# Performance work log

Hardware: AMD Instinct MI355X
Metric: run time of the kernel (lower is better)

Reference implementation:

```python
import jax, jax.numpy as jnp
import numpy as np

N = 100000  # nodes


def gcn_conv(x, src, dst, deg_inv_sqrt, W, b):
    h = x @ W  # transform first (smaller feature dim for propagation when F_out < F_in)
    norm = deg_inv_sqrt[src] * deg_inv_sqrt[dst]  # [E]
    msg = h[src] * norm[:, None]  # gather + scale
    return jax.ops.segment_sum(msg, dst, num_segments=N) + b


def setup_inputs() -> dict:
    key = jax.random.key(0)
    k1, k2, k3, k4, k5 = jax.random.split(key, 5)
    E = 3200000
    x = jax.random.normal(k1, (N, 512), dtype=jnp.float32)
    edge_index = jax.random.randint(k2, (2, E), 0, N, dtype=jnp.int64)
    W1 = jax.random.normal(k3, (512, 16), dtype=jnp.float32) * (1.0 / np.sqrt(512))
    b1 = jnp.zeros((16,), dtype=jnp.float32)
    W2 = jax.random.normal(k4, (16, 64), dtype=jnp.float32) * (1.0 / np.sqrt(16))
    b2 = jnp.zeros((64,), dtype=jnp.float32)
    return {"x": x, "edge_index": edge_index, "W1": W1, "b1": b1, "W2": W2, "b2": b2}


def reference(x, edge_index, W1, b1, W2, b2):
    # add self-loops (PyG GCNConv default add_self_loops=True)
    loops = jnp.arange(N, dtype=edge_index.dtype)
    src = jnp.concatenate([edge_index[0], loops])
    dst = jnp.concatenate([edge_index[1], loops])
    # symmetric normalization: deg computed on destination (in-degree incl. self-loop)
    deg = jax.ops.segment_sum(jnp.ones_like(dst, dtype=x.dtype), dst, num_segments=N)
    deg_inv_sqrt = jnp.where(deg > 0, jax.lax.rsqrt(jnp.maximum(deg, 1.0)), 0.0)

    h = jax.nn.relu(gcn_conv(x, src, dst, deg_inv_sqrt, W1, b1))
    out = gcn_conv(h, src, dst, deg_inv_sqrt, W2, b2)
    return jax.nn.log_softmax(out, axis=1)
```

## Files before the change

### kernel.cpp

```cpp
#include <hip/hip_runtime.h>

#define FIN 512
#define FMID 16
#define FOUT 64

typedef __attribute__((ext_vector_type(8))) short bf8_t;
typedef __attribute__((ext_vector_type(4))) float f32x4_t;

__device__ __forceinline__ unsigned short f2bf_rne(float f) {
  unsigned u = __float_as_uint(f);
  return (unsigned short)((u + 0x7FFFu + ((u >> 16) & 1u)) >> 16);
}
__device__ __forceinline__ float bf2f(unsigned short h) {
  return __uint_as_float(((unsigned)h) << 16);
}


#define CHUNK 8192

__global__ __launch_bounds__(256) void k_bhist(const int* __restrict__ dst,
                                               int* __restrict__ gtot, int E, int nbuck) {
  __shared__ int hist[1024];
  const int t = threadIdx.x;
  const int base = blockIdx.x * CHUNK;
  const int nloc = min(CHUNK, E - base);
  for (int i = t; i < nbuck; i += 256) hist[i] = 0;
  __syncthreads();
  const int nv = nloc & ~3;
  for (int i = t * 4; i < nv; i += 1024) {
    int4 d = *(const int4*)(dst + base + i);
    atomicAdd(&hist[d.x >> 8], 1);
    atomicAdd(&hist[d.y >> 8], 1);
    atomicAdd(&hist[d.z >> 8], 1);
    atomicAdd(&hist[d.w >> 8], 1);
  }
  if (t == 0)
    for (int i = nv; i < nloc; ++i) atomicAdd(&hist[dst[base + i] >> 8], 1);
  __syncthreads();
  for (int i = t; i < nbuck; i += 256) {
    int c = hist[i];
    if (c) atomicAdd(&gtot[i], c);
  }
}

__global__ __launch_bounds__(1024) void k_bscan(int* __restrict__ gbase,
                                                int* __restrict__ gcur,
                                                int* __restrict__ rowstart,
                                                int E, int n, int nbuck) {
  __shared__ int sm[1024];
  int t = threadIdx.x;
  int v = (t < nbuck) ? gbase[t] : 0;
  sm[t] = v;
  __syncthreads();
  for (int off = 1; off < 1024; off <<= 1) {
    int a = (t >= off) ? sm[t - off] : 0;
    __syncthreads();
    sm[t] += a;
    __syncthreads();
  }
  int excl = sm[t] - v;
  if (t < nbuck) {
    gbase[t] = excl;
    gcur[t] = excl;
  }
  if (t == 0) {
    gbase[nbuck] = E;
    rowstart[n] = E;
  }
}

__global__ __launch_bounds__(256) void k_bucketA(const int* __restrict__ src,
                                                 const int* __restrict__ dst,
                                                 int* __restrict__ gcur,
                                                 int* __restrict__ packed,
                                                 int E, int nbuck) {
  __shared__ int hist[1024];
  const int t = threadIdx.x;
  const int base = blockIdx.x * CHUNK;
  const int nloc = min(CHUNK, E - base);
  for (int i = t; i < nbuck; i += 256) hist[i] = 0;
  __syncthreads();
  const int nv = nloc & ~3;
  for (int i = t * 4; i < nv; i += 1024) {
    int4 d = *(const int4*)(dst + base + i);
    atomicAdd(&hist[d.x >> 8], 1);
    atomicAdd(&hist[d.y >> 8], 1);
    atomicAdd(&hist[d.z >> 8], 1);
    atomicAdd(&hist[d.w >> 8], 1);
  }
  if (t == 0)
    for (int i = nv; i < nloc; ++i) atomicAdd(&hist[dst[base + i] >> 8], 1);
  __syncthreads();
  for (int i = t; i < nbuck; i += 256) {
    int c = hist[i];
    hist[i] = c ? atomicAdd(&gcur[i], c) : 0;
  }
  __syncthreads();
  for (int i = t * 4; i < nv; i += 1024) {
    int4 d = *(const int4*)(dst + base + i);
    int4 s = *(const int4*)(src + base + i);
    int p0 = atomicAdd(&hist[d.x >> 8], 1);
    int p1 = atomicAdd(&hist[d.y >> 8], 1);
    int p2 = atomicAdd(&hist[d.z >> 8], 1);
    int p3 = atomicAdd(&hist[d.w >> 8], 1);
    packed[p0] = (s.x << 8) | (d.x & 255);
    packed[p1] = (s.y << 8) | (d.y & 255);
    packed[p2] = (s.z << 8) | (d.z & 255);
    packed[p3] = (s.w << 8) | (d.w & 255);
  }
  if (t == 0)
    for (int i = nv; i < nloc; ++i) {
      int d = dst[base + i], s = src[base + i];
      int p = atomicAdd(&hist[d >> 8], 1);
      packed[p] = (s << 8) | (d & 255);
    }
}

__global__ __launch_bounds__(256) void k_bucketB(const int* __restrict__ packed,
                                                 const int* __restrict__ gbase,
                                                 int* __restrict__ rowstart,
                                                 float* __restrict__ dis,
                                                 int* __restrict__ csr, int n) {
  __shared__ int cnt[256];
  __shared__ int cur[256];
  const int b = blockIdx.x;
  const int t = threadIdx.x;
  const int beg = gbase[b], end = gbase[b + 1];
  cnt[t] = 0;
  __syncthreads();
  for (int i = beg + t; i < end; i += 256) atomicAdd(&cnt[packed[i] & 255], 1);
  __syncthreads();
  int v = cnt[t];
  cur[t] = v;
  __syncthreads();
  for (int off = 1; off < 256; off <<= 1) {
    int a = (t >= off) ? cur[t - off] : 0;
    __syncthreads();
    cur[t] += a;
    __syncthreads();
  }
  int excl = cur[t] - v;
  int node = (b << 8) + t;
  if (node < n) {
    rowstart[node] = beg + excl;
    dis[node] = rsqrtf((float)v + 1.0f);
  }
  __syncthreads();
  cur[t] = beg + excl;
  __syncthreads();
  for (int i = beg + t; i < end; i += 256) {
    int p = packed[i];
    int pos = atomicAdd(&cur[p & 255], 1);
    csr[pos] = p >> 8;
  }
}


__global__ __launch_bounds__(256) void k_gemm1(const float* __restrict__ x,
                                               const float* __restrict__ W1,
                                               const float* __restrict__ dis,
                                               float* __restrict__ hs, int n,
                                               int ntiles) {
  __shared__ short wb_hi[16][64][8];
  __shared__ short wb_lo[16][64][8];
  for (int e = threadIdx.x; e < FIN * FMID; e += 256) {
    int k = e >> 4, j = e & 15;
    int ks = k >> 5, kk = k & 31;
    int L = ((kk >> 3) << 4) + j, i = kk & 7;
    float f = W1[e];
    unsigned short h = f2bf_rne(f);
    wb_hi[ks][L][i] = (short)h;
    wb_lo[ks][L][i] = (short)f2bf_rne(f - bf2f(h));
  }
  __syncthreads();
  const int lane = threadIdx.x & 63;
  const int wid  = threadIdx.x >> 6;
  const int rloc = lane & 15;
  const int q    = lane >> 4;
  for (int tile = blockIdx.x * 4 + wid; tile < ntiles; tile += gridDim.x * 4) {
    int row = tile * 16 + rloc;
    const float4* xr = (const float4*)(x + (size_t)(row < n ? row : n - 1) * FIN);
    f32x4_t acc = {0.f, 0.f, 0.f, 0.f};
#pragma unroll 4
    for (int ks = 0; ks < 16; ++ks) {
      float4 v0 = xr[ks * 8 + q * 2];
      float4 v1 = xr[ks * 8 + q * 2 + 1];
      float fv[8] = {v0.x, v0.y, v0.z, v0.w, v1.x, v1.y, v1.z, v1.w};
      bf8_t ah, al;
#pragma unroll
      for (int i = 0; i < 8; ++i) {
        unsigned short h = f2bf_rne(fv[i]);
        ah[i] = (short)h;
        al[i] = (short)f2bf_rne(fv[i] - bf2f(h));
      }
      bf8_t bh = *(const bf8_t*)&wb_hi[ks][lane][0];
      bf8_t bl = *(const bf8_t*)&wb_lo[ks][lane][0];
      acc = __builtin_amdgcn_mfma_f32_16x16x32_bf16(ah, bh, acc, 0, 0, 0);
      acc = __builtin_amdgcn_mfma_f32_16x16x32_bf16(al, bh, acc, 0, 0, 0);
      acc = __builtin_amdgcn_mfma_f32_16x16x32_bf16(ah, bl, acc, 0, 0, 0);
    }
    int nb = tile * 16 + q * 4;
#pragma unroll
    for (int r = 0; r < 4; ++r) {
      int node = nb + r;
      if (node < n) hs[(size_t)node * FMID + rloc] = acc[r] * dis[node];
    }
  }
}

template <bool RELU>
__global__ __launch_bounds__(256) void k_prop_csr(const float* __restrict__ hs,
                                                  const int* __restrict__ rowstart,
                                                  const int* __restrict__ csr,
                                                  const float* __restrict__ dis,
                                                  const float* __restrict__ bias,
                                                  float* __restrict__ outp, int n) {
  int t = blockIdx.x * blockDim.x + threadIdx.x;
  int node = t >> 4;
  if (node >= n) return;
  const int j = t & 15;
  const int g = j >> 2;
  const int c = j & 3;
  int beg = rowstart[node], end = rowstart[node + 1];
  float4 acc = make_float4(0.f, 0.f, 0.f, 0.f);
  if (g == 0) {
    float4 v = ((const float4*)(hs + (size_t)node * FMID))[c];
    acc.x += v.x; acc.y += v.y; acc.z += v.z; acc.w += v.w;
  }
  int i = beg;
  int stop = beg + ((end - beg) & ~15);
  for (; i < stop; i += 16) {
    int sv = csr[i + j];
#pragma unroll
    for (int k = 0; k < 4; ++k) {
      int sidx = __shfl(sv, k * 4 + g, 16);
      float4 v = ((const float4*)(hs + (size_t)sidx * FMID))[c];
      acc.x += v.x; acc.y += v.y; acc.z += v.z; acc.w += v.w;
    }
  }
  for (int u = 0; i < end; ++i, ++u) {
    int sidx = csr[i];
    if (g == (u & 3)) {
      float4 v = ((const float4*)(hs + (size_t)sidx * FMID))[c];
      acc.x += v.x; acc.y += v.y; acc.z += v.z; acc.w += v.w;
    }
  }
#pragma unroll
  for (int off = 4; off <= 8; off <<= 1) {
    acc.x += __shfl_xor(acc.x, off, 16);
    acc.y += __shfl_xor(acc.y, off, 16);
    acc.z += __shfl_xor(acc.z, off, 16);
    acc.w += __shfl_xor(acc.w, off, 16);
  }
  if (g == 0) {
    float dd = dis[node];
    float4 r;
    r.x = dd * acc.x; r.y = dd * acc.y; r.z = dd * acc.z; r.w = dd * acc.w;
    if (RELU) {
      float4 bb = ((const float4*)bias)[c];
      r.x = fmaxf(r.x + bb.x, 0.f) * dd;
      r.y = fmaxf(r.y + bb.y, 0.f) * dd;
      r.z = fmaxf(r.z + bb.z, 0.f) * dd;
      r.w = fmaxf(r.w + bb.w, 0.f) * dd;
    }
    ((float4*)(outp + (size_t)node * FMID))[c] = r;
  }
}

__global__ __launch_bounds__(256) void k_out(const float* __restrict__ a2,
                                             const float* __restrict__ W2,
                                             const float* __restrict__ b2,
                                             float* __restrict__ out, int n) {
  __shared__ float w[FMID * FOUT];
  for (int idx = threadIdx.x; idx < FMID * FOUT; idx += 256) w[idx] = W2[idx];
  __syncthreads();
  const int lane = threadIdx.x & 63;
  const int node = blockIdx.x * 4 + (threadIdx.x >> 6);
  if (node >= n) return;
  const float* ar = a2 + (size_t)node * FMID;
  float o = b2[lane];
#pragma unroll
  for (int k = 0; k < FMID; ++k) o += ar[k] * w[k * FOUT + lane];
  float m = o;
#pragma unroll
  for (int off = 32; off >= 1; off >>= 1) m = fmaxf(m, __shfl_xor(m, off));
  float e = __expf(o - m);
  float s = e;
#pragma unroll
  for (int off = 32; off >= 1; off >>= 1) s += __shfl_xor(s, off);
  out[(size_t)node * FOUT + lane] = o - m - __logf(s);
}


__global__ void k_deg_init(float* __restrict__ deg, int n) {
  int i = blockIdx.x * blockDim.x + threadIdx.x;
  if (i < n) deg[i] = 1.0f;
}
__global__ void k_deg_edges(const int* __restrict__ dst, float* __restrict__ deg, int E) {
  int e = blockIdx.x * blockDim.x + threadIdx.x;
  if (e < E) atomicAdd(&deg[dst[e]], 1.0f);
}
__global__ void k_deg_finish(float* __restrict__ deg, int n) {
  int i = blockIdx.x * blockDim.x + threadIdx.x;
  if (i < n) deg[i] = rsqrtf(deg[i]);
}
__global__ void k_selfloop_s(const float* __restrict__ hs, const float* __restrict__ dis,
                             float* __restrict__ a, int total16) {
  int t = blockIdx.x * blockDim.x + threadIdx.x;
  if (t < total16) a[t] = hs[t] * dis[t >> 4];
}
__global__ void k_prop_atomic(const float* __restrict__ hs, const int* __restrict__ src,
                              const int* __restrict__ dst, const float* __restrict__ dis,
                              float* __restrict__ outp, int E) {
  int t = blockIdx.x * blockDim.x + threadIdx.x;
  int e = t >> 4;
  if (e >= E) return;
  int jj = t & 15;
  int s = src[e], d = dst[e];
  atomicAdd(&outp[(size_t)d * FMID + jj], hs[(size_t)s * FMID + jj] * dis[d]);
}
__global__ void k_bias_relu_s(float* __restrict__ a, const float* __restrict__ b,
                              const float* __restrict__ dis, int total16) {
  int t = blockIdx.x * blockDim.x + threadIdx.x;
  if (t < total16) {
    float v = a[t] + b[t & 15];
    a[t] = (v > 0.f ? v : 0.f) * dis[t >> 4];
  }
}


extern "C" void kernel_launch(void* const* d_in, const int* in_sizes, int n_in,
                              void* d_out, int out_size, void* d_ws, size_t ws_size,
                              hipStream_t stream) {
  const float* x  = (const float*)d_in[0];
  const int* edge = (const int*)d_in[1];
  const float* W1 = (const float*)d_in[2];
  const float* b1 = (const float*)d_in[3];
  const float* W2 = (const float*)d_in[4];
  const float* b2 = (const float*)d_in[5];
  float* out = (float*)d_out;

  const int N = in_sizes[0] / FIN;
  const int E = in_sizes[1] / 2;
  const int* src = edge;
  const int* dst = edge + E;

  const int T = 256;
  const int t16n = N * FMID;
  const int ntiles = (N + 15) / 16;
  int gblocks = (ntiles + 3) / 4;
  if (gblocks > 2048) gblocks = 2048;

  const int nbuck = (N + 255) >> 8;
  const int nblkA = (E + CHUNK - 1) / CHUNK;

  size_t need_csr = ((size_t)33 * N + (size_t)(N + 1) + (size_t)(2 * nbuck + 1) +
                     (size_t)E) * 4;
  bool new_ok = (ws_size >= need_csr) && ((size_t)E <= (size_t)32 * N) &&
                (nbuck <= 1024) && ((size_t)N < (1u << 23));

  if (new_ok) {
    float* fbase = (float*)d_ws;
    float* dis  = fbase;
    float* buf0 = fbase + (size_t)N;
    float* buf1 = fbase + 17 * (size_t)N;
    int* packed   = (int*)buf0;
    int* ibase    = (int*)(fbase + 33 * (size_t)N);
    int* rowstart = ibase;
    int* gbase    = ibase + (size_t)N + 1;
    int* gcur     = gbase + nbuck + 1;
    int* csr      = gcur + nbuck;

    hipMemsetAsync(gbase, 0, (size_t)(nbuck + 1) * sizeof(int), stream);
    k_bhist  <<<nblkA, T, 0, stream>>>(dst, gbase, E, nbuck);
    k_bscan  <<<1, 1024, 0, stream>>>(gbase, gcur, rowstart, E, N, nbuck);
    k_bucketA<<<nblkA, T, 0, stream>>>(src, dst, gcur, packed, E, nbuck);
    k_bucketB<<<nbuck, T, 0, stream>>>(packed, gbase, rowstart, dis, csr, N);

    k_gemm1  <<<gblocks, T, 0, stream>>>(x, W1, dis, buf0, N, ntiles);

    const int PB = (t16n + T - 1) / T;
    k_prop_csr<true>  <<<PB, T, 0, stream>>>(buf0, rowstart, csr, dis, b1, buf1, N);
    k_prop_csr<false> <<<PB, T, 0, stream>>>(buf1, rowstart, csr, dis, b1, buf0, N);
    k_out    <<<(N + 3) / 4, T, 0, stream>>>(buf0, W2, b2, out, N);
  } else {
    float* f   = (float*)d_ws;
    float* dis = f;
    float* hs  = f + (size_t)N;
    float* a1  = f + 17 * (size_t)N;
    float* a2  = f + 33 * (size_t)N;
    const long te = (long)E * FMID;

    k_deg_init  <<<(N + T - 1) / T, T, 0, stream>>>(dis, N);
    k_deg_edges <<<(E + T - 1) / T, T, 0, stream>>>(dst, dis, E);
    k_deg_finish<<<(N + T - 1) / T, T, 0, stream>>>(dis, N);

    k_gemm1     <<<gblocks, T, 0, stream>>>(x, W1, dis, hs, N, ntiles);

    k_selfloop_s<<<(t16n + T - 1) / T, T, 0, stream>>>(hs, dis, a1, t16n);
    k_prop_atomic<<<(int)((te + T - 1) / T), T, 0, stream>>>(hs, src, dst, dis, a1, E);
    k_bias_relu_s<<<(t16n + T - 1) / T, T, 0, stream>>>(a1, b1, dis, t16n);

    k_selfloop_s<<<(t16n + T - 1) / T, T, 0, stream>>>(a1, dis, a2, t16n);
    k_prop_atomic<<<(int)((te + T - 1) / T), T, 0, stream>>>(a1, src, dst, dis, a2, E);

    k_out       <<<(N + 3) / 4, T, 0, stream>>>(a2, W2, b2, out, N);
  }
}
```

Before: 548.6 us.

## Switch CSR propagation to edge-parallel blocks with shared-memory atomic accumulation

The CSR array now keeps the packed (src<<8 | local dst) word, so propagation can run edge-parallel over each 64-node block's contiguous edge range. Each edge's 4-float chunk is gathered and added into a shared-memory accumulator with LDS atomics, replacing the node-per-16-lane loop that suffered from load imbalance and partial tail iterations. This trades warp divergence and degree imbalance for LDS atomic contention and extra block syncs. The output kernel also loads each node's 16 features as four float4 vectors instead of scalar reads.

```diff
diff --git a/kernel.cpp b/kernel.cpp
--- a/kernel.cpp
+++ b/kernel.cpp
@@ -151,7 +151,7 @@
   for (int i = beg + t; i < end; i += 256) {
     int p = packed[i];
     int pos = atomicAdd(&cur[p & 255], 1);
-    csr[pos] = p >> 8;
+    csr[pos] = p;
   }
 }
 
@@ -209,53 +209,47 @@
 }
 
 template <bool RELU>
-__global__ __launch_bounds__(256) void k_prop_csr(const float* __restrict__ hs,
-                                                  const int* __restrict__ rowstart,
-                                                  const int* __restrict__ csr,
-                                                  const float* __restrict__ dis,
-                                                  const float* __restrict__ bias,
-                                                  float* __restrict__ outp, int n) {
-  int t = blockIdx.x * blockDim.x + threadIdx.x;
-  int node = t >> 4;
-  if (node >= n) return;
-  const int j = t & 15;
-  const int g = j >> 2;
-  const int c = j & 3;
-  int beg = rowstart[node], end = rowstart[node + 1];
-  float4 acc = make_float4(0.f, 0.f, 0.f, 0.f);
-  if (g == 0) {
-    float4 v = ((const float4*)(hs + (size_t)node * FMID))[c];
-    acc.x += v.x; acc.y += v.y; acc.z += v.z; acc.w += v.w;
-  }
-  int i = beg;
-  int stop = beg + ((end - beg) & ~15);
-  for (; i < stop; i += 16) {
-    int sv = csr[i + j];
-#pragma unroll
-    for (int k = 0; k < 4; ++k) {
-      int sidx = __shfl(sv, k * 4 + g, 16);
-      float4 v = ((const float4*)(hs + (size_t)sidx * FMID))[c];
-      acc.x += v.x; acc.y += v.y; acc.z += v.z; acc.w += v.w;
+__global__ __launch_bounds__(256) void k_prop_ep(const float* __restrict__ hs,
+                                                 const int* __restrict__ rowstart,
+                                                 const int* __restrict__ csrp,
+                                                 const float* __restrict__ dis,
+                                                 const float* __restrict__ bias,
+                                                 float* __restrict__ outp, int n) {
+  __shared__ float acc[64][16];
+  const int t = threadIdx.x;
+  const int node0 = blockIdx.x * 64;
+  const int nl = t >> 2;
+  const int c  = t & 3;
+  const int node = node0 + nl;
+  float4 selfv = make_float4(0.f, 0.f, 0.f, 0.f);
+  if (node < n) selfv = ((const float4*)hs)[(size_t)node * 4 + c];
+  *(float4*)&acc[nl][c * 4] = selfv;
+  __syncthreads();
+  const int beg = rowstart[node0];
+  const int end = rowstart[min(node0 + 64, n)];
+  const int es = t >> 2;
+  for (int base = beg; base < end; base += 256) {
+#pragma unroll
+    for (int u = 0; u < 4; ++u) {
+      int i = base + u * 64 + es;
+      if (i < end) {
+        int p = csrp[i];
+        int s = p >> 8;
+        int dl = p & 63;
+        float4 v = ((const float4*)hs)[(size_t)s * 4 + c];
+        atomicAdd(&acc[dl][c * 4 + 0], v.x);
+        atomicAdd(&acc[dl][c * 4 + 1], v.y);
+        atomicAdd(&acc[dl][c * 4 + 2], v.z);
+        atomicAdd(&acc[dl][c * 4 + 3], v.w);
+      }
     }
   }
-  for (int u = 0; i < end; ++i, ++u) {
-    int sidx = csr[i];
-    if (g == (u & 3)) {
-      float4 v = ((const float4*)(hs + (size_t)sidx * FMID))[c];
-      acc.x += v.x; acc.y += v.y; acc.z += v.z; acc.w += v.w;
-    }
-  }
-#pragma unroll
-  for (int off = 4; off <= 8; off <<= 1) {
-    acc.x += __shfl_xor(acc.x, off, 16);
-    acc.y += __shfl_xor(acc.y, off, 16);
-    acc.z += __shfl_xor(acc.z, off, 16);
-    acc.w += __shfl_xor(acc.w, off, 16);
-  }
-  if (g == 0) {
+  __syncthreads();
+  if (node < n) {
     float dd = dis[node];
+    float4 a = *(const float4*)&acc[nl][c * 4];
     float4 r;
-    r.x = dd * acc.x; r.y = dd * acc.y; r.z = dd * acc.z; r.w = dd * acc.w;
+    r.x = dd * a.x; r.y = dd * a.y; r.z = dd * a.z; r.w = dd * a.w;
     if (RELU) {
       float4 bb = ((const float4*)bias)[c];
       r.x = fmaxf(r.x + bb.x, 0.f) * dd;
@@ -263,7 +257,7 @@
       r.z = fmaxf(r.z + bb.z, 0.f) * dd;
       r.w = fmaxf(r.w + bb.w, 0.f) * dd;
     }
-    ((float4*)(outp + (size_t)node * FMID))[c] = r;
+    ((float4*)outp)[(size_t)node * 4 + c] = r;
   }
 }
 
@@ -277,10 +271,13 @@
   const int lane = threadIdx.x & 63;
   const int node = blockIdx.x * 4 + (threadIdx.x >> 6);
   if (node >= n) return;
-  const float* ar = a2 + (size_t)node * FMID;
+  const float4* ar4 = (const float4*)(a2 + (size_t)node * FMID);
+  float4 q0 = ar4[0], q1 = ar4[1], q2 = ar4[2], q3 = ar4[3];
+  float av[16] = {q0.x, q0.y, q0.z, q0.w, q1.x, q1.y, q1.z, q1.w,
+                  q2.x, q2.y, q2.z, q2.w, q3.x, q3.y, q3.z, q3.w};
   float o = b2[lane];
 #pragma unroll
-  for (int k = 0; k < FMID; ++k) o += ar[k] * w[k * FOUT + lane];
+  for (int k = 0; k < FMID; ++k) o += av[k] * w[k * FOUT + lane];
   float m = o;
 #pragma unroll
   for (int off = 32; off >= 1; off >>= 1) m = fmaxf(m, __shfl_xor(m, off));
@@ -353,6 +350,7 @@
 
   const int nbuck = (N + 255) >> 8;
   const int nblkA = (E + CHUNK - 1) / CHUNK;
+  const int nblk64 = (N + 63) / 64;
 
   size_t need_csr = ((size_t)33 * N + (size_t)(N + 1) + (size_t)(2 * nbuck + 1) +
                      (size_t)E) * 4;
@@ -379,9 +377,8 @@
 
     k_gemm1  <<<gblocks, T, 0, stream>>>(x, W1, dis, buf0, N, ntiles);
 
-    const int PB = (t16n + T - 1) / T;
-    k_prop_csr<true>  <<<PB, T, 0, stream>>>(buf0, rowstart, csr, dis, b1, buf1, N);
-    k_prop_csr<false> <<<PB, T, 0, stream>>>(buf1, rowstart, csr, dis, b1, buf0, N);
+    k_prop_ep<true>  <<<nblk64, T, 0, stream>>>(buf0, rowstart, csr, dis, b1, buf1, N);
+    k_prop_ep<false> <<<nblk64, T, 0, stream>>>(buf1, rowstart, csr, dis, b1, buf0, N);
     k_out    <<<(N + 3) / 4, T, 0, stream>>>(buf0, W2, b2, out, N);
   } else {
     float* f   = (float*)d_ws;
```

New measurement: 1.032 ms. 1.88x slower.
